# Kernel optimization log

Measured on AMD Instinct MI355X. Metric: run time of the kernel, lower is better.

## Reference

```python
import jax, jax.numpy as jnp
import numpy as np

B, T, V, E, DC, H = 128, 25, 10000, 512, 512, 512
N0 = H + E + DC  # layer-0 concat width
N1 = 2 * H       # layer-1 concat width


def setup_inputs() -> dict:
    key = jax.random.key(0)
    ks = jax.random.split(key, 12)
    def w(k, n):
        return jax.random.normal(k, (n, H), dtype=jnp.float32) / np.float32(np.sqrt(n))
    return {
        "tokens": jax.random.randint(ks[0], (B, T), 0, V),
        "processed_cnn_features": jax.random.normal(ks[1], (B, DC), dtype=jnp.float32),
        "initial_hidden_state": jnp.zeros((2, B, H), dtype=jnp.float32),
        "embedding": jax.random.normal(ks[2], (V, E), dtype=jnp.float32) * 0.1,
        "Wu0": w(ks[3], N0), "Wr0": w(ks[4], N0), "Wc0": w(ks[5], N0),
        "bu0": jnp.zeros((H,), jnp.float32), "br0": jnp.zeros((H,), jnp.float32), "bc0": jnp.zeros((H,), jnp.float32),
        "Wu1": w(ks[6], N1), "Wr1": w(ks[7], N1), "Wc1": w(ks[8], N1),
        "bu1": jnp.zeros((H,), jnp.float32), "br1": jnp.zeros((H,), jnp.float32), "bc1": jnp.zeros((H,), jnp.float32),
        "Wout": jax.random.normal(ks[9], (H, V), dtype=jnp.float32) / np.float32(np.sqrt(H)),
        "bout": jnp.zeros((V,), jnp.float32),
    }


def gru_step(x, h, Wu, bu, Wr, br, Wc, bc):
    xh = jnp.concatenate([x, h], axis=1)
    u = jax.nn.sigmoid(xh @ Wu + bu)
    r = jax.nn.sigmoid(xh @ Wr + br)
    cand = jnp.tanh(jnp.concatenate([x, r * h], axis=1) @ Wc + bc)
    return u * h + (1.0 - u) * cand


def reference(tokens, processed_cnn_features, initial_hidden_state, embedding,
              Wu0, Wr0, Wc0, bu0, br0, bc0,
              Wu1, Wr1, Wc1, bu1, br1, bc1,
              Wout, bout):
    emb = embedding[tokens]              # [B, T, E]
    emb_t = jnp.transpose(emb, (1, 0, 2))  # [T, B, E]

    def step(carry, e_t):
        h0, h1 = carry
        x0 = jnp.concatenate([e_t, processed_cnn_features], axis=1)  # [B, E+DC]
        h0 = gru_step(x0, h0, Wu0, bu0, Wr0, br0, Wc0, bc0)
        h1 = gru_step(h0, h1, Wu1, bu1, Wr1, br1, Wc1, bc1)
        logits = h1 @ Wout + bout  # [B, V]
        return (h0, h1), logits

    (h0, h1), logits_seq = jax.lax.scan(step, (initial_hidden_state[0], initial_hidden_state[1]), emb_t)
    logits = jnp.transpose(logits_seq, (1, 0, 2))  # [B, T, V]
    final_hidden = jnp.stack([h0, h1])             # [2, B, H]
    return logits, final_hidden
```

## Files before the change

### kernel.cpp

```cpp
#include <hip/hip_runtime.h>

#define T_ 25
#define V_ 10000
#define NWG_ 192

#define R_P1 0
#define R_P2 1
#define R_P3 2
#define R_P4 3

typedef short bf16x8 __attribute__((ext_vector_type(8)));
typedef float f32x4 __attribute__((ext_vector_type(4)));

__device__ __forceinline__ short f2bf(float x) {
  union { float f; unsigned u; } v; v.f = x;
  unsigned r = (v.u + 0x7fffu + ((v.u >> 16) & 1u)) >> 16;
  return (short)r;
}
__device__ __forceinline__ float sigm(float z) { return 1.f / (1.f + __expf(-z)); }
__device__ __forceinline__ float tanhfast(float z) {
  float e = __expf(2.f * z);
  return 1.f - 2.f / (e + 1.f);
}

__device__ __forceinline__ void gload_lds16(const void* g, void* l) {
  __builtin_amdgcn_global_load_lds((const __attribute__((address_space(1))) void*)g,
                                   (__attribute__((address_space(3))) void*)l, 16, 0, 0);
}

__device__ __forceinline__ void vwait0() { asm volatile("s_waitcnt vmcnt(0)" ::: "memory"); }
__device__ __forceinline__ void vwait_n(int n) {
  switch (n) {
    case 0:  asm volatile("s_waitcnt vmcnt(0)"  ::: "memory"); break;
    case 8:  asm volatile("s_waitcnt vmcnt(8)"  ::: "memory"); break;
    case 16: asm volatile("s_waitcnt vmcnt(16)" ::: "memory"); break;
    default: asm volatile("s_waitcnt vmcnt(0)"  ::: "memory"); break;
  }
}
__device__ __forceinline__ void cload16(bf16x8* d, const short* p) {
  asm volatile("global_load_dwordx4 %0, %1, off sc0 sc1" : "=v"(*d) : "v"(p) : "memory");
}
__device__ __forceinline__ void cloadf(float* d, const float* p) {
  asm volatile("global_load_dword %0, %1, off sc0 sc1" : "=v"(*d) : "v"(p) : "memory");
}
__device__ __forceinline__ void cstoref(float* p, float v) {
  asm volatile("global_store_dword %0, %1, off sc0 sc1" :: "v"(p), "v"(v) : "memory");
}
__device__ __forceinline__ void cstores(short* p, int v) {
  asm volatile("global_store_short %0, %1, off sc0 sc1" :: "v"(p), "v"(v) : "memory");
}

__device__ __forceinline__ int FL(int row, int col) {
  return (((col >> 5) * 8 + (row >> 4)) << 9) | (((row & 15) | (((col >> 3) & 3) << 4)) << 3) | (col & 7);
}

__device__ __forceinline__ void arrive(int* bar, int role, int rep) {
  vwait0();
  __syncthreads();
  if (threadIdx.x == 0)
    __hip_atomic_fetch_add(&bar[(role * 8 + rep) * 32], 1, __ATOMIC_RELAXED, __HIP_MEMORY_SCOPE_AGENT);
}
__device__ __forceinline__ int rsum(int* bar, int role) {
  int s = 0;
#pragma unroll
  for (int r = 0; r < 8; r++)
    s += __hip_atomic_load(&bar[(role * 8 + r) * 32], __ATOMIC_RELAXED, __HIP_MEMORY_SCOPE_AGENT);
  return s;
}
__device__ __forceinline__ void waitc(int* bar, int r0, int n0, int r1, int n1, int r2, int n2) {
  if (threadIdx.x == 0) {
    for (;;) {
      bool ok = true;
      if (r0 >= 0 && rsum(bar, r0) < n0) ok = false;
      if (ok && r1 >= 0 && rsum(bar, r1) < n1) ok = false;
      if (ok && r2 >= 0 && rsum(bar, r2) < n2) ok = false;
      if (ok) break;
      __builtin_amdgcn_s_sleep(2);
    }
  }
  __syncthreads();
}

struct TJob { const float* src; short* dst; int R, C, t0; };
struct TJobs { TJob j[10]; };

__global__ void tcast_all(TJobs J) {
  __shared__ float t[32][33];
  int bid = blockIdx.x;
  int ji = 0;
  while (ji < 9 && bid >= J.j[ji + 1].t0) ji++;
  const float* src = J.j[ji].src;
  short* dst = J.j[ji].dst;
  int R = J.j[ji].R, C = J.j[ji].C;
  int rel = bid - J.j[ji].t0;
  int ctiles = (C + 31) >> 5;
  int rt0 = (rel / ctiles) * 32, ct0 = (rel % ctiles) * 32;
  int tx = threadIdx.x, ty = threadIdx.y;
#pragma unroll
  for (int i = 0; i < 4; i++) {
    int r = rt0 + ty + i * 8, c = ct0 + tx;
    if (r < R && c < C) t[ty + i * 8][tx] = src[(size_t)r * C + c];
  }
  __syncthreads();
#pragma unroll
  for (int i = 0; i < 4; i++) {
    int c = ct0 + ty + i * 8, r = rt0 + tx;
    if (r < R && c < C) dst[(size_t)c * R + r] = f2bf(t[tx][ty + i * 8]);
  }
}

__global__ void build_x0(const int* __restrict__ tok, const float* __restrict__ emb,
                         const float* __restrict__ cnn, short* __restrict__ X0) {
  int row = blockIdx.x;
  int t = row >> 7, b = row & 127;
  int tk = tok[b * T_ + t];
  const float* er = emb + (size_t)tk * 512;
  short* dst = X0 + (size_t)row * 1024;
  for (int i = threadIdx.x; i < 1024; i += 256)
    dst[i] = f2bf(i < 512 ? er[i] : cnn[b * 512 + (i - 512)]);
}

__global__ void init_h(const float* __restrict__ ihs, float* h0f, float* h1f,
                       short* xh1b0, short* xh1b1) {
  int i = blockIdx.x * 256 + threadIdx.x;
  if (i < 65536) {
    int b = i >> 9, h = i & 511;
    float v0 = ihs[i], v1 = ihs[65536 + i];
    h0f[i] = v0; h1f[i] = v1;
    xh1b1[FL(b, h)] = f2bf(v0);
    xh1b0[FL(b, 512 + h)] = f2bf(v1);
  }
}

struct RP {
  short *xh1b0, *xh1b1, *rh0b, *xc1b0, *xc1b1, *H1all;
  float *u0f, *u1f, *h0f, *h1f;
  const float *A0;
  const short *Whur0T, *Whc0T, *W1urT, *Wc1T;
  const float *bu1, *br1, *bc1;
  float *outp;
  int *bar;
};

template<int NKS>
__device__ __forceinline__ void wload(const short* __restrict__ Wt, int n0, int lane, bf16x8* wfr) {
  const short* p = Wt + (size_t)(n0 + (lane & 15)) * (NKS * 32) + ((lane >> 4) * 8);
#pragma unroll
  for (int ks = 0; ks < NKS; ks++) wfr[ks] = *(const bf16x8*)(p + (size_t)ks * 32);
}

template<int NKS>
__device__ __forceinline__ void kcompute_coh(const short* __restrict__ A, int rb0, int lane,
                                             const bf16x8* __restrict__ wfr, f32x4* acc) {
  const short* ap = A + rb0 * 512 + lane * 8;
  constexpr int NCH = NKS / 4;
  constexpr int DEPTH = NCH < 3 ? NCH : 3;
  bf16x8 s0[4][4], s1[4][4];
#pragma unroll
  for (int c = 0; c < DEPTH; c++)
#pragma unroll
    for (int j = 0; j < 4; j++) {
      cload16(&s0[c & 3][j], ap + (c * 4 + j) * 4096);
      cload16(&s1[c & 3][j], ap + (c * 4 + j) * 4096 + 512);
    }
#pragma unroll
  for (int c = 0; c < NCH; c++) {
    const int issued = (DEPTH + c < NCH) ? DEPTH + c : NCH;
    vwait_n((issued - c - 1) * 8);
    __builtin_amdgcn_sched_barrier(0);
#pragma unroll
    for (int j = 0; j < 4; j++) {
      int ks = c * 4 + j;
      acc[ks & 1]       = __builtin_amdgcn_mfma_f32_16x16x32_bf16(s0[c & 3][j], wfr[ks], acc[ks & 1], 0, 0, 0);
      acc[2 + (ks & 1)] = __builtin_amdgcn_mfma_f32_16x16x32_bf16(s1[c & 3][j], wfr[ks], acc[2 + (ks & 1)], 0, 0, 0);
    }
    if (DEPTH + c < NCH) {
      const int nc = DEPTH + c;
#pragma unroll
      for (int j = 0; j < 4; j++) {
        cload16(&s0[nc & 3][j], ap + (nc * 4 + j) * 4096);
        cload16(&s1[nc & 3][j], ap + (nc * 4 + j) * 4096 + 512);
      }
    }
  }
}

__global__ __launch_bounds__(256, 1) void recurrence(RP p) {
  const int role = blockIdx.x;
  const int tid = threadIdx.x, wv = tid >> 6, lane = tid & 63;
  const int lr = lane & 15, lg = lane >> 4;
  int* bar = p.bar;

  if (role < 64) {
    const int widx = role, rep = widx & 7;
    const int nt = widx >> 1, mh = widx & 1;
    const int colb = nt * 32 + (wv & 1) * 16;
    const int rb0 = mh * 4 + (wv >> 1) * 2;
    const int col = colb + lr;
    bf16x8 wfr[32]; wload<32>(p.W1urT, colb, lane, wfr);
    for (int s = 0; s < T_; s++) {
      waitc(bar, R_P2, 32 * (s + 1), s >= 1 ? R_P4 : -1, 32 * s, -1, 0);
      const short* A = (s & 1) ? p.xh1b1 : p.xh1b0;
      float hv[8];
      if (colb >= 512) {
#pragma unroll
        for (int m = 0; m < 2; m++)
#pragma unroll
          for (int i = 0; i < 4; i++)
            cloadf(&hv[m * 4 + i], &p.h1f[((rb0 + m) * 16 + lg * 4 + i) * 512 + (col - 512)]);
      }
      f32x4 acc[4] = {};
      kcompute_coh<32>(A, rb0, lane, wfr, acc);
      f32x4 am[2] = { acc[0] + acc[1], acc[2] + acc[3] };
      short* xc = (s & 1) ? p.xc1b1 : p.xc1b0;
      if (colb < 512) {
#pragma unroll
        for (int m = 0; m < 2; m++)
#pragma unroll
          for (int i = 0; i < 4; i++) {
            int row = (rb0 + m) * 16 + lg * 4 + i;
            cstoref(&p.u1f[row * 512 + col], sigm(am[m][i] + p.bu1[col]));
          }
      } else {
#pragma unroll
        for (int m = 0; m < 2; m++)
#pragma unroll
          for (int i = 0; i < 4; i++) {
            int row = (rb0 + m) * 16 + lg * 4 + i;
            float sg = sigm(am[m][i] + p.br1[col - 512]);
            cstores(&xc[FL(row, col)], f2bf(sg * hv[m * 4 + i]));
          }
      }
      arrive(bar, R_P3, rep);
    }
  } else if (role < 128) {
    const int widx = role - 64, rep = widx & 7;
    const int nt = widx >> 1, mh = widx & 1;
    const int colb = nt * 32 + (wv & 1) * 16;
    const int rb0 = mh * 4 + (wv >> 1) * 2;
    const int col = colb + lr;
    bf16x8 wfr[16]; wload<16>(p.Whur0T, colb, lane, wfr);
    for (int s = 0; s < T_; s++) {
      waitc(bar, s >= 1 ? R_P2 : -1, 32 * s, -1, 0, -1, 0);
      const short* A = (s & 1) ? p.xh1b0 : p.xh1b1;
      float hv[8];
      if (colb >= 512) {
#pragma unroll
        for (int m = 0; m < 2; m++)
#pragma unroll
          for (int i = 0; i < 4; i++)
            cloadf(&hv[m * 4 + i], &p.h0f[((rb0 + m) * 16 + lg * 4 + i) * 512 + (col - 512)]);
      }
      f32x4 acc[4] = {};
      kcompute_coh<16>(A, rb0, lane, wfr, acc);
      f32x4 am[2] = { acc[0] + acc[1], acc[2] + acc[3] };
      const float* a0s = p.A0 + (size_t)s * 196608;
      if (colb < 512) {
#pragma unroll
        for (int m = 0; m < 2; m++)
#pragma unroll
          for (int i = 0; i < 4; i++) {
            int row = (rb0 + m) * 16 + lg * 4 + i;
            cstoref(&p.u0f[row * 512 + col], sigm(am[m][i] + a0s[row * 1536 + col]));
          }
      } else {
#pragma unroll
        for (int m = 0; m < 2; m++)
#pragma unroll
          for (int i = 0; i < 4; i++) {
            int row = (rb0 + m) * 16 + lg * 4 + i;
            float sg = sigm(am[m][i] + a0s[row * 1536 + col]);
            cstores(&p.rh0b[FL(row, col - 512)], f2bf(sg * hv[m * 4 + i]));
          }
      }
      arrive(bar, R_P1, rep);
    }
  } else if (role < 160) {
    const int widx = role - 128, rep = widx & 7;
    const int nt = widx >> 1, mh = widx & 1;
    const int colb = nt * 32 + (wv & 1) * 16;
    const int rb0 = mh * 4 + (wv >> 1) * 2;
    const int col = colb + lr;
    bf16x8 wfr[32]; wload<32>(p.Wc1T, colb, lane, wfr);
    for (int s = 0; s < T_; s++) {
      waitc(bar, R_P3, 64 * (s + 1), R_P2, 32 * (s + 1), -1, 0);
      const short* xc = (s & 1) ? p.xc1b1 : p.xc1b0;
      float uv[8], hv[8];
#pragma unroll
      for (int m = 0; m < 2; m++)
#pragma unroll
        for (int i = 0; i < 4; i++) {
          int row = (rb0 + m) * 16 + lg * 4 + i;
          cloadf(&uv[m * 4 + i], &p.u1f[row * 512 + col]);
          cloadf(&hv[m * 4 + i], &p.h1f[row * 512 + col]);
        }
      f32x4 acc[4] = {};
      kcompute_coh<32>(xc, rb0, lane, wfr, acc);
      f32x4 am[2] = { acc[0] + acc[1], acc[2] + acc[3] };
      short* xh = (s & 1) ? p.xh1b0 : p.xh1b1;
#pragma unroll
      for (int m = 0; m < 2; m++)
#pragma unroll
        for (int i = 0; i < 4; i++) {
          int row = (rb0 + m) * 16 + lg * 4 + i;
          float cc = tanhfast(am[m][i] + p.bc1[col]);
          float u = uv[m * 4 + i], h = hv[m * 4 + i];
          float hn = u * h + (1.f - u) * cc;
          cstoref(&p.h1f[row * 512 + col], hn);
          short hb = f2bf(hn);
          cstores(&xh[FL(row, 512 + col)], hb);
          p.H1all[(size_t)s * 65536 + row * 512 + col] = hb;
          if (s == T_ - 1) p.outp[32000000 + 65536 + row * 512 + col] = hn;
        }
      arrive(bar, R_P4, rep);
    }
  } else {
    const int widx = role - 160, rep = widx & 7;
    const int nt = widx >> 1, mh = widx & 1;
    const int colb = nt * 32 + (wv & 1) * 16;
    const int rb0 = mh * 4 + (wv >> 1) * 2;
    const int col = colb + lr;
    bf16x8 wfr[16]; wload<16>(p.Whc0T, colb, lane, wfr);
    for (int s = 0; s < T_; s++) {
      waitc(bar, R_P1, 64 * (s + 1), s >= 1 ? R_P3 : -1, 64 * (s - 1),
            s >= 2 ? R_P4 : -1, 32 * (s - 1));
      float uv[8], hv[8];
#pragma unroll
      for (int m = 0; m < 2; m++)
#pragma unroll
        for (int i = 0; i < 4; i++) {
          int row = (rb0 + m) * 16 + lg * 4 + i;
          cloadf(&uv[m * 4 + i], &p.u0f[row * 512 + col]);
          cloadf(&hv[m * 4 + i], &p.h0f[row * 512 + col]);
        }
      f32x4 acc[4] = {};
      kcompute_coh<16>(p.rh0b, rb0, lane, wfr, acc);
      f32x4 am[2] = { acc[0] + acc[1], acc[2] + acc[3] };
      const float* a0s = p.A0 + (size_t)s * 196608;
      short* xh  = (s & 1) ? p.xh1b1 : p.xh1b0;
      short* xcw = (s & 1) ? p.xc1b1 : p.xc1b0;
#pragma unroll
      for (int m = 0; m < 2; m++)
#pragma unroll
        for (int i = 0; i < 4; i++) {
          int row = (rb0 + m) * 16 + lg * 4 + i;
          float c = tanhfast(am[m][i] + a0s[row * 1536 + 1024 + col]);
          float u = uv[m * 4 + i], h = hv[m * 4 + i];
          float hn = u * h + (1.f - u) * c;
          cstoref(&p.h0f[row * 512 + col], hn);
          short hb = f2bf(hn);
          cstores(&xh[FL(row, col)], hb);
          cstores(&xcw[FL(row, col)], hb);
          if (s == T_ - 1) p.outp[32000000 + row * 512 + col] = hn;
        }
      arrive(bar, R_P2, rep);
    }
  }
}

struct GP {
  const short* A; const short* Bt;
  int lda, ldb, N, K;
  const float* bias0; const float* bias1; const float* bias2;
  float* fdst;
  float* outp; const float* bout;
};

template<int BM, int BN, int VAR>
__device__ __forceinline__ void gemm_core(const GP& p, short* la, short* lb, int bm, int bn, short* smem) {
  const int tid = threadIdx.x;
  const int wave = tid >> 6, lane = tid & 63;
  const int wm = wave >> 1, wn = wave & 1;
  constexpr int WM = BM / 2, WN = BN / 2;
  constexpr int MF = WM / 16, NF = WN / 16;
  const int lr = lane & 15, lg = lane >> 4;
  const short* Abase = p.A + (size_t)bm * BM * p.lda;
  const short* Bbase = p.Bt + (size_t)bn * BN * p.ldb;
  const int bnmax = p.N - bn * BN;
  f32x4 acc[MF][NF] = {};
  const int nkb = p.K >> 6;

  auto stA = [&](int buf, int k0) {
    constexpr int NI = BM / 32;
#pragma unroll
    for (int j = 0; j < NI; j++) {
      int glin = j * 256 + tid;
      int row = glin >> 3, gc = glin & 7;
      int gcs = gc ^ (row & 7);
      gload_lds16(Abase + (size_t)row * p.lda + k0 + gcs * 8,
                  &la[buf * BM * 64 + j * 2048 + wave * 512]);
    }
  };
  auto stB = [&](int buf, int k0) {
    constexpr int NI = BN / 32;
#pragma unroll
    for (int j = 0; j < NI; j++) {
      int glin = j * 256 + tid;
      int row = glin >> 3, gc = glin & 7;
      int gcs = gc ^ (row & 7);
      int rc = row < bnmax ? row : bnmax - 1;
      gload_lds16(Bbase + (size_t)rc * p.ldb + k0 + gcs * 8,
                  &lb[buf * BN * 64 + j * 2048 + wave * 512]);
    }
  };

  stA(0, 0); stB(0, 0);
  __syncthreads();
  int buf = 0;
  for (int kb = 0; kb < nkb; kb++) {
    if (kb + 1 < nkb) { stA(buf ^ 1, (kb + 1) * 64); stB(buf ^ 1, (kb + 1) * 64); }
    bf16x8 af[2][MF], bfr[2][NF];
#pragma unroll
    for (int ks = 0; ks < 2; ks++) {
#pragma unroll
      for (int m = 0; m < MF; m++) {
        int ar = wm * WM + m * 16 + lr;
        af[ks][m] = *(const bf16x8*)&la[buf * BM * 64 + (ar * 8 + ((ks * 4 + lg) ^ (ar & 7))) * 8];
      }
#pragma unroll
      for (int n = 0; n < NF; n++) {
        int br = wn * WN + n * 16 + lr;
        bfr[ks][n] = *(const bf16x8*)&lb[buf * BN * 64 + (br * 8 + ((ks * 4 + lg) ^ (br & 7))) * 8];
      }
    }
#pragma unroll
    for (int ks = 0; ks < 2; ks++)
#pragma unroll
      for (int m = 0; m < MF; m++)
#pragma unroll
        for (int n = 0; n < NF; n++)
          acc[m][n] = __builtin_amdgcn_mfma_f32_16x16x32_bf16(af[ks][m], bfr[ks][n], acc[m][n], 0, 0, 0);
    __syncthreads();
    buf ^= 1;
  }

  if constexpr (VAR == 0) {
#pragma unroll
    for (int m = 0; m < MF; m++)
#pragma unroll
      for (int n = 0; n < NF; n++)
#pragma unroll
        for (int i = 0; i < 4; i++) {
          int row = bm * BM + wm * WM + m * 16 + lg * 4 + i;
          int col = bn * BN + wn * WN + n * 16 + lr;
          if (col >= p.N) continue;
          float bias = col < 512 ? p.bias0[col] : (col < 1024 ? p.bias1[col - 512] : p.bias2[col - 1024]);
          p.fdst[(size_t)row * 1536 + col] = acc[m][n][i] + bias;
        }
  } else {
    float* fs = (float*)smem;
#pragma unroll
    for (int m = 0; m < MF; m++)
#pragma unroll
      for (int n = 0; n < NF; n++)
#pragma unroll
        for (int i = 0; i < 4; i++) {
          int lrow = wm * WM + m * 16 + lg * 4 + i;
          int lcol = wn * WN + n * 16 + lr;
          int col = bn * BN + lcol;
          fs[lrow * 128 + lcol] = acc[m][n][i] + (col < p.N ? p.bout[col] : 0.f);
        }
    __syncthreads();
#pragma unroll
    for (int j = 0; j < 16; j++) {
      int idx = j * 256 + tid;
      int r = idx >> 5, c4 = (idx & 31) << 2;
      int gr = bm * BM + r;
      int tt = gr >> 7, b = gr & 127;
      int col = bn * BN + c4;
      if (col < p.N) {
        f32x4 v = *(const f32x4*)&fs[r * 128 + c4];
        *(f32x4*)&p.outp[((size_t)b * T_ + tt) * V_ + col] = v;
      }
    }
  }
}

template<int BM, int BN, int VAR>
__global__ __launch_bounds__(256) void gemm_one(GP p) {
  __shared__ short smem[2 * BM * 64 + 2 * BN * 64];
  int bm, bn;
  if constexpr (VAR == 5) {
    int lin = blockIdx.y * gridDim.x + blockIdx.x;
    const int nwg = 79 * 25, q = nwg / 8, r8 = nwg % 8;
    int xcd = lin % 8, idx = lin / 8;
    int nlin = (xcd < r8 ? xcd * (q + 1) : r8 * (q + 1) + (xcd - r8) * q) + idx;
    bm = nlin % 25; bn = nlin / 25;
  } else { bm = blockIdx.y; bn = blockIdx.x; }
  gemm_core<BM, BN, VAR>(p, smem, smem + 2 * BM * 64, bm, bn, smem);
}

extern "C" void kernel_launch(void* const* d_in, const int* in_sizes, int n_in,
                              void* d_out, int out_size, void* d_ws, size_t ws_size,
                              hipStream_t stream) {
  const int*   tokens = (const int*)  d_in[0];
  const float* cnn    = (const float*)d_in[1];
  const float* ihs    = (const float*)d_in[2];
  const float* emb    = (const float*)d_in[3];
  const float* Wu0 = (const float*)d_in[4];
  const float* Wr0 = (const float*)d_in[5];
  const float* Wc0 = (const float*)d_in[6];
  const float* bu0 = (const float*)d_in[7];
  const float* br0 = (const float*)d_in[8];
  const float* bc0 = (const float*)d_in[9];
  const float* Wu1 = (const float*)d_in[10];
  const float* Wr1 = (const float*)d_in[11];
  const float* Wc1 = (const float*)d_in[12];
  const float* bu1 = (const float*)d_in[13];
  const float* br1 = (const float*)d_in[14];
  const float* bc1 = (const float*)d_in[15];
  const float* Wout = (const float*)d_in[16];
  const float* bout = (const float*)d_in[17];
  float* out = (float*)d_out;

  char* w = (char*)d_ws;
  size_t off = 0;
  auto alloc = [&](size_t bytes) { void* p = w + off; off += (bytes + 255) & ~255ull; return p; };
  short* WxT    = (short*)alloc(1536 * 1024 * 2);
  short* Whur0T = (short*)alloc(1024 * 512 * 2);
  short* Whc0T  = (short*)alloc(512 * 512 * 2);
  short* W1urT  = (short*)alloc(1024 * 1024 * 2);
  short* Wc1T   = (short*)alloc(512 * 1024 * 2);
  short* WoutT  = (short*)alloc((size_t)10000 * 512 * 2);
  short* X0     = (short*)alloc((size_t)3200 * 1024 * 2);
  float* A0     = (float*)alloc((size_t)3200 * 1536 * 4);
  short* H1all  = (short*)alloc((size_t)3200 * 512 * 2);
  float* u0f    = (float*)alloc(128 * 512 * 4);
  float* u1f    = (float*)alloc(128 * 512 * 4);
  float* h0f    = (float*)alloc(128 * 512 * 4);
  float* h1f    = (float*)alloc(128 * 512 * 4);
  short* rh0b   = (short*)alloc(128 * 512 * 2);
  short* xh1b0  = (short*)alloc(128 * 1024 * 2);
  short* xh1b1  = (short*)alloc(128 * 1024 * 2);
  short* xc1b0  = (short*)alloc(128 * 1024 * 2);
  short* xc1b1  = (short*)alloc(128 * 1024 * 2);
  int*   bar    = (int*)alloc(4096);
  (void)ws_size; (void)in_sizes; (void)n_in; (void)out_size;

  {
    TJobs J;
    J.j[0] = { Wu0,              WxT,                1024, 512,  0    };
    J.j[1] = { Wr0,              WxT + 512 * 1024,   1024, 512,  512  };
    J.j[2] = { Wc0,              WxT + 1024 * 1024,  1024, 512,  1024 };
    J.j[3] = { Wu0 + 1024 * 512, Whur0T,             512,  512,  1536 };
    J.j[4] = { Wr0 + 1024 * 512, Whur0T + 512 * 512, 512,  512,  1792 };
    J.j[5] = { Wc0 + 1024 * 512, Whc0T,              512,  512,  2048 };
    J.j[6] = { Wu1,              W1urT,              1024, 512,  2304 };
    J.j[7] = { Wr1,              W1urT + 512 * 1024, 1024, 512,  2816 };
    J.j[8] = { Wc1,              Wc1T,               1024, 512,  3328 };
    J.j[9] = { Wout,             WoutT,              512,  10000, 3840 };
    tcast_all<<<8848, dim3(32, 8), 0, stream>>>(J);
  }

  build_x0<<<3200, 256, 0, stream>>>(tokens, emb, cnn, X0);
  init_h<<<256, 256, 0, stream>>>(ihs, h0f, h1f, xh1b0, xh1b1);
  hipMemsetAsync(bar, 0, 4096, stream);

  {
    GP g = {};
    g.A = X0; g.lda = 1024; g.Bt = WxT; g.ldb = 1024; g.N = 1536; g.K = 1024;
    g.bias0 = bu0; g.bias1 = br0; g.bias2 = bc0; g.fdst = A0;
    gemm_one<128, 128, 0><<<dim3(12, 25), 256, 0, stream>>>(g);
  }

  {
    RP r = {};
    r.xh1b0 = xh1b0; r.xh1b1 = xh1b1; r.rh0b = rh0b; r.xc1b0 = xc1b0; r.xc1b1 = xc1b1;
    r.H1all = H1all;
    r.u0f = u0f; r.u1f = u1f; r.h0f = h0f; r.h1f = h1f;
    r.A0 = A0;
    r.Whur0T = Whur0T; r.Whc0T = Whc0T; r.W1urT = W1urT; r.Wc1T = Wc1T;
    r.bu1 = bu1; r.br1 = br1; r.bc1 = bc1;
    r.outp = out;
    r.bar = bar;
    recurrence<<<dim3(NWG_), 256, 0, stream>>>(r);
  }

  {
    GP g = {};
    g.A = H1all; g.lda = 512; g.Bt = WoutT; g.ldb = 512; g.N = 10000; g.K = 512;
    g.outp = out; g.bout = bout;
    gemm_one<128, 128, 5><<<dim3(79, 25), 256, 0, stream>>>(g);
  }
}
```

Before: 548.9 us.

## Use per-timestep recurrence buffers to drop WAR barriers and use non-coherent loads

Replaces the ping-pong hidden, candidate and gate buffers with a separate buffer slice per timestep. Each slice is written once, so the waits that guarded against overwriting data still in use by earlier steps are removed, and the MFMA operand loads drop the sc0/sc1 coherence bits. The four roles are also interleaved across block IDs, which changes how they map to XCDs, and the spin-wait sleep is shortened. The cost is a larger workspace, and correctness now relies on never-read-before addresses not being stale in non-coherent caches across XCDs.

Measured after the change: 534.2 us, median of 2. 1.03x faster.

```diff
diff --git a/kernel.cpp b/kernel.cpp
--- a/kernel.cpp
+++ b/kernel.cpp
@@ -4,10 +4,10 @@
 #define V_ 10000
 #define NWG_ 192
 
-#define R_P1 0
-#define R_P2 1
-#define R_P3 2
-#define R_P4 3
+#define R_P3 0
+#define R_P1 1
+#define R_P4 2
+#define R_P2 3
 
 typedef short bf16x8 __attribute__((ext_vector_type(8)));
 typedef float f32x4 __attribute__((ext_vector_type(4)));
@@ -37,11 +37,8 @@
     default: asm volatile("s_waitcnt vmcnt(0)"  ::: "memory"); break;
   }
 }
-__device__ __forceinline__ void cload16(bf16x8* d, const short* p) {
-  asm volatile("global_load_dwordx4 %0, %1, off sc0 sc1" : "=v"(*d) : "v"(p) : "memory");
-}
-__device__ __forceinline__ void cloadf(float* d, const float* p) {
-  asm volatile("global_load_dword %0, %1, off sc0 sc1" : "=v"(*d) : "v"(p) : "memory");
+__device__ __forceinline__ void ncload16(bf16x8* d, const short* p) {
+  asm volatile("global_load_dwordx4 %0, %1, off" : "=v"(*d) : "v"(p) : "memory");
 }
 __device__ __forceinline__ void cstoref(float* p, float v) {
   asm volatile("global_store_dword %0, %1, off sc0 sc1" :: "v"(p), "v"(v) : "memory");
@@ -67,15 +64,14 @@
     s += __hip_atomic_load(&bar[(role * 8 + r) * 32], __ATOMIC_RELAXED, __HIP_MEMORY_SCOPE_AGENT);
   return s;
 }
-__device__ __forceinline__ void waitc(int* bar, int r0, int n0, int r1, int n1, int r2, int n2) {
+__device__ __forceinline__ void waitc(int* bar, int r0, int n0, int r1, int n1) {
   if (threadIdx.x == 0) {
     for (;;) {
       bool ok = true;
       if (r0 >= 0 && rsum(bar, r0) < n0) ok = false;
       if (ok && r1 >= 0 && rsum(bar, r1) < n1) ok = false;
-      if (ok && r2 >= 0 && rsum(bar, r2) < n2) ok = false;
       if (ok) break;
-      __builtin_amdgcn_s_sleep(2);
+      __builtin_amdgcn_s_sleep(1);
     }
   }
   __syncthreads();
@@ -120,21 +116,20 @@
     dst[i] = f2bf(i < 512 ? er[i] : cnn[b * 512 + (i - 512)]);
 }
 
-__global__ void init_h(const float* __restrict__ ihs, float* h0f, float* h1f,
-                       short* xh1b0, short* xh1b1) {
+__global__ void init_h(const float* __restrict__ ihs, float* h0f0, float* h1f0, short* H0) {
   int i = blockIdx.x * 256 + threadIdx.x;
   if (i < 65536) {
     int b = i >> 9, h = i & 511;
     float v0 = ihs[i], v1 = ihs[65536 + i];
-    h0f[i] = v0; h1f[i] = v1;
-    xh1b1[FL(b, h)] = f2bf(v0);
-    xh1b0[FL(b, 512 + h)] = f2bf(v1);
+    h0f0[i] = v0; h1f0[i] = v1;
+    H0[FL(b, h)] = f2bf(v0);
+    H0[FL(b, 512 + h)] = f2bf(v1);
   }
 }
 
 struct RP {
-  short *xh1b0, *xh1b1, *rh0b, *xc1b0, *xc1b1, *H1all;
-  float *u0f, *u1f, *h0f, *h1f;
+  short *Hb, *XCb, *RHb, *H1all;
+  float *u0b, *u1b, *h0b, *h1b;
   const float *A0;
   const short *Whur0T, *Whc0T, *W1urT, *Wc1T;
   const float *bu1, *br1, *bc1;
@@ -149,10 +144,11 @@
   for (int ks = 0; ks < NKS; ks++) wfr[ks] = *(const bf16x8*)(p + (size_t)ks * 32);
 }
 
-template<int NKS>
-__device__ __forceinline__ void kcompute_coh(const short* __restrict__ A, int rb0, int lane,
-                                             const bf16x8* __restrict__ wfr, f32x4* acc) {
-  const short* ap = A + rb0 * 512 + lane * 8;
+template<int NKS, bool SPLIT>
+__device__ __forceinline__ void kcompute(const short* __restrict__ Alo, const short* __restrict__ Ahi,
+                                         int rb0, int lane, const bf16x8* __restrict__ wfr, f32x4* acc) {
+  const short* aplo = Alo + rb0 * 512 + lane * 8;
+  const short* aphi = Ahi + rb0 * 512 + lane * 8;
   constexpr int NCH = NKS / 4;
   constexpr int DEPTH = NCH < 3 ? NCH : 3;
   bf16x8 s0[4][4], s1[4][4];
@@ -160,8 +156,10 @@
   for (int c = 0; c < DEPTH; c++)
 #pragma unroll
     for (int j = 0; j < 4; j++) {
-      cload16(&s0[c & 3][j], ap + (c * 4 + j) * 4096);
-      cload16(&s1[c & 3][j], ap + (c * 4 + j) * 4096 + 512);
+      int ks = c * 4 + j;
+      const short* ap = (SPLIT && ks >= NKS / 2) ? aphi : aplo;
+      ncload16(&s0[c & 3][j], ap + ks * 4096);
+      ncload16(&s1[c & 3][j], ap + ks * 4096 + 512);
     }
 #pragma unroll
   for (int c = 0; c < NCH; c++) {
@@ -178,135 +176,102 @@
       const int nc = DEPTH + c;
 #pragma unroll
       for (int j = 0; j < 4; j++) {
-        cload16(&s0[nc & 3][j], ap + (nc * 4 + j) * 4096);
-        cload16(&s1[nc & 3][j], ap + (nc * 4 + j) * 4096 + 512);
+        int ks = nc * 4 + j;
+        const short* ap = (SPLIT && ks >= NKS / 2) ? aphi : aplo;
+        ncload16(&s0[nc & 3][j], ap + ks * 4096);
+        ncload16(&s1[nc & 3][j], ap + ks * 4096 + 512);
       }
     }
   }
 }
 
 __global__ __launch_bounds__(256, 1) void recurrence(RP p) {
-  const int role = blockIdx.x;
+  const int bid = blockIdx.x;
+  const int m8 = bid & 7;
+  const int k = ((bid & 127) >> 3) * 4 + (m8 & 3);
+  const int role = (bid < 128) ? ((m8 < 4) ? R_P3 : R_P1) : ((m8 < 4) ? R_P4 : R_P2);
+  const int rep = k & 7;
   const int tid = threadIdx.x, wv = tid >> 6, lane = tid & 63;
   const int lr = lane & 15, lg = lane >> 4;
   int* bar = p.bar;
-
-  if (role < 64) {
-    const int widx = role, rep = widx & 7;
-    const int nt = widx >> 1, mh = widx & 1;
-    const int colb = nt * 32 + (wv & 1) * 16;
-    const int rb0 = mh * 4 + (wv >> 1) * 2;
-    const int col = colb + lr;
+  const int nt = k >> 1, mh = k & 1;
+  const int colb = nt * 32 + (wv & 1) * 16;
+  const int rb0 = mh * 4 + (wv >> 1) * 2;
+  const int col = colb + lr;
+
+  if (role == R_P3) {
     bf16x8 wfr[32]; wload<32>(p.W1urT, colb, lane, wfr);
     for (int s = 0; s < T_; s++) {
-      waitc(bar, R_P2, 32 * (s + 1), s >= 1 ? R_P4 : -1, 32 * s, -1, 0);
-      const short* A = (s & 1) ? p.xh1b1 : p.xh1b0;
-      float hv[8];
-      if (colb >= 512) {
-#pragma unroll
-        for (int m = 0; m < 2; m++)
-#pragma unroll
-          for (int i = 0; i < 4; i++)
-            cloadf(&hv[m * 4 + i], &p.h1f[((rb0 + m) * 16 + lg * 4 + i) * 512 + (col - 512)]);
-      }
+      waitc(bar, R_P2, 32 * (s + 1), s >= 1 ? R_P4 : -1, 32 * s);
+      const short* Hs1 = p.Hb + (size_t)(s + 1) * 131072;
+      const short* Hs  = p.Hb + (size_t)s * 131072;
       f32x4 acc[4] = {};
-      kcompute_coh<32>(A, rb0, lane, wfr, acc);
+      kcompute<32, true>(Hs1, Hs, rb0, lane, wfr, acc);
       f32x4 am[2] = { acc[0] + acc[1], acc[2] + acc[3] };
-      short* xc = (s & 1) ? p.xc1b1 : p.xc1b0;
-      if (colb < 512) {
-#pragma unroll
-        for (int m = 0; m < 2; m++)
-#pragma unroll
-          for (int i = 0; i < 4; i++) {
-            int row = (rb0 + m) * 16 + lg * 4 + i;
-            cstoref(&p.u1f[row * 512 + col], sigm(am[m][i] + p.bu1[col]));
+      short* xc = p.XCb + (size_t)s * 131072;
+      const float* h1s = p.h1b + (size_t)s * 65536;
+      float* u1s = p.u1b + (size_t)s * 65536;
+#pragma unroll
+      for (int m = 0; m < 2; m++)
+#pragma unroll
+        for (int i = 0; i < 4; i++) {
+          int row = (rb0 + m) * 16 + lg * 4 + i;
+          if (colb < 512) {
+            cstoref(&u1s[row * 512 + col], sigm(am[m][i] + p.bu1[col]));
+          } else {
+            float sg = sigm(am[m][i] + p.br1[col - 512]);
+            cstores(&xc[FL(row, col)], f2bf(sg * h1s[row * 512 + (col - 512)]));
           }
-      } else {
-#pragma unroll
-        for (int m = 0; m < 2; m++)
-#pragma unroll
-          for (int i = 0; i < 4; i++) {
-            int row = (rb0 + m) * 16 + lg * 4 + i;
-            float sg = sigm(am[m][i] + p.br1[col - 512]);
-            cstores(&xc[FL(row, col)], f2bf(sg * hv[m * 4 + i]));
-          }
-      }
+        }
       arrive(bar, R_P3, rep);
     }
-  } else if (role < 128) {
-    const int widx = role - 64, rep = widx & 7;
-    const int nt = widx >> 1, mh = widx & 1;
-    const int colb = nt * 32 + (wv & 1) * 16;
-    const int rb0 = mh * 4 + (wv >> 1) * 2;
-    const int col = colb + lr;
+  } else if (role == R_P1) {
     bf16x8 wfr[16]; wload<16>(p.Whur0T, colb, lane, wfr);
     for (int s = 0; s < T_; s++) {
-      waitc(bar, s >= 1 ? R_P2 : -1, 32 * s, -1, 0, -1, 0);
-      const short* A = (s & 1) ? p.xh1b0 : p.xh1b1;
-      float hv[8];
-      if (colb >= 512) {
-#pragma unroll
-        for (int m = 0; m < 2; m++)
-#pragma unroll
-          for (int i = 0; i < 4; i++)
-            cloadf(&hv[m * 4 + i], &p.h0f[((rb0 + m) * 16 + lg * 4 + i) * 512 + (col - 512)]);
-      }
+      if (s >= 1) waitc(bar, R_P2, 32 * s, -1, 0);
+      const short* Hs = p.Hb + (size_t)s * 131072;
       f32x4 acc[4] = {};
-      kcompute_coh<16>(A, rb0, lane, wfr, acc);
+      kcompute<16, false>(Hs, Hs, rb0, lane, wfr, acc);
       f32x4 am[2] = { acc[0] + acc[1], acc[2] + acc[3] };
       const float* a0s = p.A0 + (size_t)s * 196608;
-      if (colb < 512) {
-#pragma unroll
-        for (int m = 0; m < 2; m++)
-#pragma unroll
-          for (int i = 0; i < 4; i++) {
-            int row = (rb0 + m) * 16 + lg * 4 + i;
-            cstoref(&p.u0f[row * 512 + col], sigm(am[m][i] + a0s[row * 1536 + col]));
+      const float* h0s = p.h0b + (size_t)s * 65536;
+      float* u0s = p.u0b + (size_t)s * 65536;
+      short* rh = p.RHb + (size_t)s * 65536;
+#pragma unroll
+      for (int m = 0; m < 2; m++)
+#pragma unroll
+        for (int i = 0; i < 4; i++) {
+          int row = (rb0 + m) * 16 + lg * 4 + i;
+          if (colb < 512) {
+            cstoref(&u0s[row * 512 + col], sigm(am[m][i] + a0s[row * 1536 + col]));
+          } else {
+            float sg = sigm(am[m][i] + a0s[row * 1536 + col]);
+            cstores(&rh[FL(row, col - 512)], f2bf(sg * h0s[row * 512 + (col - 512)]));
           }
-      } else {
-#pragma unroll
-        for (int m = 0; m < 2; m++)
-#pragma unroll
-          for (int i = 0; i < 4; i++) {
-            int row = (rb0 + m) * 16 + lg * 4 + i;
-            float sg = sigm(am[m][i] + a0s[row * 1536 + col]);
-            cstores(&p.rh0b[FL(row, col - 512)], f2bf(sg * hv[m * 4 + i]));
-          }
-      }
+        }
       arrive(bar, R_P1, rep);
     }
-  } else if (role < 160) {
-    const int widx = role - 128, rep = widx & 7;
-    const int nt = widx >> 1, mh = widx & 1;
-    const int colb = nt * 32 + (wv & 1) * 16;
-    const int rb0 = mh * 4 + (wv >> 1) * 2;
-    const int col = colb + lr;
+  } else if (role == R_P4) {
     bf16x8 wfr[32]; wload<32>(p.Wc1T, colb, lane, wfr);
     for (int s = 0; s < T_; s++) {
-      waitc(bar, R_P3, 64 * (s + 1), R_P2, 32 * (s + 1), -1, 0);
-      const short* xc = (s & 1) ? p.xc1b1 : p.xc1b0;
-      float uv[8], hv[8];
-#pragma unroll
-      for (int m = 0; m < 2; m++)
-#pragma unroll
-        for (int i = 0; i < 4; i++) {
-          int row = (rb0 + m) * 16 + lg * 4 + i;
-          cloadf(&uv[m * 4 + i], &p.u1f[row * 512 + col]);
-          cloadf(&hv[m * 4 + i], &p.h1f[row * 512 + col]);
-        }
+      waitc(bar, R_P3, 64 * (s + 1), R_P2, 32 * (s + 1));
+      const short* xc = p.XCb + (size_t)s * 131072;
       f32x4 acc[4] = {};
-      kcompute_coh<32>(xc, rb0, lane, wfr, acc);
+      kcompute<32, false>(xc, xc, rb0, lane, wfr, acc);
       f32x4 am[2] = { acc[0] + acc[1], acc[2] + acc[3] };
-      short* xh = (s & 1) ? p.xh1b0 : p.xh1b1;
+      const float* u1s = p.u1b + (size_t)s * 65536;
+      const float* h1s = p.h1b + (size_t)s * 65536;
+      float* h1d = p.h1b + (size_t)(s + 1) * 65536;
+      short* xh = p.Hb + (size_t)(s + 1) * 131072;
 #pragma unroll
       for (int m = 0; m < 2; m++)
 #pragma unroll
         for (int i = 0; i < 4; i++) {
           int row = (rb0 + m) * 16 + lg * 4 + i;
           float cc = tanhfast(am[m][i] + p.bc1[col]);
-          float u = uv[m * 4 + i], h = hv[m * 4 + i];
+          float u = u1s[row * 512 + col], h = h1s[row * 512 + col];
           float hn = u * h + (1.f - u) * cc;
-          cstoref(&p.h1f[row * 512 + col], hn);
+          cstoref(&h1d[row * 512 + col], hn);
           short hb = f2bf(hn);
           cstores(&xh[FL(row, 512 + col)], hb);
           p.H1all[(size_t)s * 65536 + row * 512 + col] = hb;
@@ -315,39 +280,28 @@
       arrive(bar, R_P4, rep);
     }
   } else {
-    const int widx = role - 160, rep = widx & 7;
-    const int nt = widx >> 1, mh = widx & 1;
-    const int colb = nt * 32 + (wv & 1) * 16;
-    const int rb0 = mh * 4 + (wv >> 1) * 2;
-    const int col = colb + lr;
     bf16x8 wfr[16]; wload<16>(p.Whc0T, colb, lane, wfr);
     for (int s = 0; s < T_; s++) {
-      waitc(bar, R_P1, 64 * (s + 1), s >= 1 ? R_P3 : -1, 64 * (s - 1),
-            s >= 2 ? R_P4 : -1, 32 * (s - 1));
-      float uv[8], hv[8];
-#pragma unroll
-      for (int m = 0; m < 2; m++)
-#pragma unroll
-        for (int i = 0; i < 4; i++) {
-          int row = (rb0 + m) * 16 + lg * 4 + i;
-          cloadf(&uv[m * 4 + i], &p.u0f[row * 512 + col]);
-          cloadf(&hv[m * 4 + i], &p.h0f[row * 512 + col]);
-        }
+      waitc(bar, R_P1, 64 * (s + 1), -1, 0);
+      const short* rh = p.RHb + (size_t)s * 65536;
       f32x4 acc[4] = {};
-      kcompute_coh<16>(p.rh0b, rb0, lane, wfr, acc);
+      kcompute<16, false>(rh, rh, rb0, lane, wfr, acc);
       f32x4 am[2] = { acc[0] + acc[1], acc[2] + acc[3] };
       const float* a0s = p.A0 + (size_t)s * 196608;
-      short* xh  = (s & 1) ? p.xh1b1 : p.xh1b0;
-      short* xcw = (s & 1) ? p.xc1b1 : p.xc1b0;
+      const float* u0s = p.u0b + (size_t)s * 65536;
+      const float* h0s = p.h0b + (size_t)s * 65536;
+      float* h0d = p.h0b + (size_t)(s + 1) * 65536;
+      short* xh  = p.Hb + (size_t)(s + 1) * 131072;
+      short* xcw = p.XCb + (size_t)s * 131072;
 #pragma unroll
       for (int m = 0; m < 2; m++)
 #pragma unroll
         for (int i = 0; i < 4; i++) {
           int row = (rb0 + m) * 16 + lg * 4 + i;
           float c = tanhfast(am[m][i] + a0s[row * 1536 + 1024 + col]);
-          float u = uv[m * 4 + i], h = hv[m * 4 + i];
+          float u = u0s[row * 512 + col], h = h0s[row * 512 + col];
           float hn = u * h + (1.f - u) * c;
-          cstoref(&p.h0f[row * 512 + col], hn);
+          cstoref(&h0d[row * 512 + col], hn);
           short hb = f2bf(hn);
           cstores(&xh[FL(row, col)], hb);
           cstores(&xcw[FL(row, col)], hb);
@@ -525,15 +479,13 @@
   short* X0     = (short*)alloc((size_t)3200 * 1024 * 2);
   float* A0     = (float*)alloc((size_t)3200 * 1536 * 4);
   short* H1all  = (short*)alloc((size_t)3200 * 512 * 2);
-  float* u0f    = (float*)alloc(128 * 512 * 4);
-  float* u1f    = (float*)alloc(128 * 512 * 4);
-  float* h0f    = (float*)alloc(128 * 512 * 4);
-  float* h1f    = (float*)alloc(128 * 512 * 4);
-  short* rh0b   = (short*)alloc(128 * 512 * 2);
-  short* xh1b0  = (short*)alloc(128 * 1024 * 2);
-  short* xh1b1  = (short*)alloc(128 * 1024 * 2);
-  short* xc1b0  = (short*)alloc(128 * 1024 * 2);
-  short* xc1b1  = (short*)alloc(128 * 1024 * 2);
+  short* Hb     = (short*)alloc((size_t)26 * 131072 * 2);
+  short* XCb    = (short*)alloc((size_t)25 * 131072 * 2);
+  short* RHb    = (short*)alloc((size_t)25 * 65536 * 2);
+  float* u0b    = (float*)alloc((size_t)25 * 65536 * 4);
+  float* u1b    = (float*)alloc((size_t)25 * 65536 * 4);
+  float* h0b    = (float*)alloc((size_t)26 * 65536 * 4);
+  float* h1b    = (float*)alloc((size_t)26 * 65536 * 4);
   int*   bar    = (int*)alloc(4096);
   (void)ws_size; (void)in_sizes; (void)n_in; (void)out_size;
 
@@ -553,7 +505,7 @@
   }
 
   build_x0<<<3200, 256, 0, stream>>>(tokens, emb, cnn, X0);
-  init_h<<<256, 256, 0, stream>>>(ihs, h0f, h1f, xh1b0, xh1b1);
+  init_h<<<256, 256, 0, stream>>>(ihs, h0b, h1b, Hb);
   hipMemsetAsync(bar, 0, 4096, stream);
 
   {
@@ -565,9 +517,8 @@
 
   {
     RP r = {};
-    r.xh1b0 = xh1b0; r.xh1b1 = xh1b1; r.rh0b = rh0b; r.xc1b0 = xc1b0; r.xc1b1 = xc1b1;
-    r.H1all = H1all;
-    r.u0f = u0f; r.u1f = u1f; r.h0f = h0f; r.h1f = h1f;
+    r.Hb = Hb; r.XCb = XCb; r.RHb = RHb; r.H1all = H1all;
+    r.u0b = u0b; r.u1b = u1b; r.h0b = h0b; r.h1b = h1b;
     r.A0 = A0;
     r.Whur0T = Whur0T; r.Whc0T = Whc0T; r.W1urT = W1urT; r.Wc1T = Wc1T;
     r.bu1 = bu1; r.br1 = br1; r.bc1 = bc1;
```
